# Optimization experiments

Hardware: AMD Instinct MI355X
Metric: run time of the kernel (lower is better)

The kernel has to match this reference:

```python
import jax, jax.numpy as jnp
import numpy as np

M = 16            # num_frequencies
DIM = 512         # dim_input
B = 32768         # flattened batch
H = M + 1         # raw complex table side
N = 2 * M + 1     # autocorrelated table side
NPAR = H * H      # (m+1)^2


def setup_inputs() -> dict:
    key = jax.random.key(0)
    k1, k2, k3 = jax.random.split(key, 3)
    inputs = jax.random.normal(k1, (B, DIM), dtype=jnp.float32)
    targets = jax.random.uniform(k2, (B, 2), dtype=jnp.float32)  # points in [0,1) subset of [-1,1]^2
    # nn.init.normal_(weight, 0.01) => mean=0.01, std=1.0 ; bias zeros
    W = jax.random.normal(k3, (2 * NPAR, DIM), dtype=jnp.float32) + 0.01
    b = jnp.zeros((2 * NPAR,), dtype=jnp.float32)
    return {"inputs": inputs, "targets": targets, "W": W, "b": b}


def reference(inputs, targets, W, b):
    # Linear -> unconstrained complex (m+1)x(m+1) table per sample
    p = inputs @ W.T + b                                   # (B, 2*NPAR)
    real = p[:, :NPAR].reshape(-1, H, H)
    imag = p[:, NPAR:].reshape(-1, H, H)
    seq = jax.lax.complex(real, imag)                      # (B, H, H) complex64

    # 2D linear autocorrelation r[tau] = sum_i seq[i+tau] * conj(seq[i]),
    # tau in [-M, M]^2, via zero-padded FFT (equivalent to the grouped conv2d).
    F = jnp.fft.fft2(seq, s=(N, N))                        # (B, N, N)
    ac = jnp.fft.ifft2(F * jnp.conj(F))                    # circular autocorr
    ac = jnp.roll(ac, (M, M), axis=(-2, -1))               # index a -> lag a-M

    # Normalize so C[0,0] (= centre) equals 1/4 => unit mass on [-1,1]^2
    centre = ac[:, M, M].real                              # sum |seq|^2 > 0
    C = ac / (4.0 * centre)[:, None, None]                 # (B, N, N)

    # Evaluate f(x,y) = sum_{kx,ky} C * exp(i*pi*(kx*x + ky*y))
    k = jnp.arange(-M, M + 1, dtype=jnp.float32)
    kx, ky = jnp.meshgrid(k, k, indexing='xy')             # (N, N)
    tx = targets[:, 0][:, None, None]
    ty = targets[:, 1][:, None, None]
    phase = kx[None] * tx + ky[None] * ty                  # (B, N, N)
    exps = jnp.exp(1j * jnp.pi * phase)
    pdf = jnp.einsum('bij,bij->b', C, exps).real           # (B,)
    return pdf
```

## Files before the change

kernel.cpp:

```cpp
#include <hip/hip_runtime.h>

#define NPARC 289
#define NOUT  578
#define DIMK  512
#define CTILES 40
#define BATCH 32768

typedef __bf16 bf16x8 __attribute__((ext_vector_type(8)));
typedef float floatx4 __attribute__((ext_vector_type(4)));

__device__ __forceinline__ unsigned short f2bf(float f) {
    unsigned u = __float_as_uint(f);
    u = (u + 0x7fffu + ((u >> 16) & 1u)) >> 16;
    return (unsigned short)u;
}

__global__ void prep_w(const float* __restrict__ W, unsigned short* __restrict__ Wp) {
    int wid = threadIdx.x >> 6;
    int lane = threadIdx.x & 63;
    int col = blockIdx.x * 4 + wid;
    int k = lane * 8;
    unsigned short v[8];
    if (col < NOUT) {
        const float* src = W + (size_t)col * DIMK + k;
        #pragma unroll
        for (int j = 0; j < 8; ++j) v[j] = f2bf(src[j]);
    } else {
        #pragma unroll
        for (int j = 0; j < 8; ++j) v[j] = 0;
    }
    int ct = col >> 4;
    int ks = k >> 5;
    int ln = (((k >> 3) & 3) << 4) + (col & 15);
    uint4 o;
    o.x = (unsigned)v[0] | ((unsigned)v[1] << 16);
    o.y = (unsigned)v[2] | ((unsigned)v[3] << 16);
    o.z = (unsigned)v[4] | ((unsigned)v[5] << 16);
    o.w = (unsigned)v[6] | ((unsigned)v[7] << 16);
    *(uint4*)(Wp + (size_t)((ct * 16 + ks) * 64 + ln) * 8) = o;
}

__global__ __launch_bounds__(512, 4) void fused_kernel(
    const float* __restrict__ inputs, const float* __restrict__ targets,
    const float* __restrict__ bias, const unsigned short* __restrict__ Wp,
    float* __restrict__ out)
{
    __shared__ __align__(16) unsigned short Alds[64 * 64 * 8];
    const int tid = threadIdx.x;
    const int base = blockIdx.x * 64;

    const float4* inp4 = (const float4*)(inputs + (size_t)base * DIMK);
    #pragma unroll
    for (int i = 0; i < 16; ++i) {
        int f = i * 512 + tid;
        int s = f >> 7;
        int k = (f & 127) * 4;
        float4 v = inp4[f];
        int t = ((s >> 4) << 4) + (k >> 5);
        int ln = ((((k >> 3) & 3) << 4) + (s & 15)) ^ (t & 7);
        int off = (t * 64 + ln) * 8 + (k & 7);
        union { __bf16 h[4]; uint2 u; } cv;
        cv.h[0] = (__bf16)v.x; cv.h[1] = (__bf16)v.y;
        cv.h[2] = (__bf16)v.z; cv.h[3] = (__bf16)v.w;
        *(uint2*)&Alds[off] = cv.u;
    }
    __syncthreads();

    const int wid  = tid >> 6;
    const int lane = tid & 63;
    const int quad = lane >> 4;
    const int lcol = lane & 15;

    floatx4 acc[5][4];
    #pragma unroll
    for (int t5 = 0; t5 < 5; ++t5)
        #pragma unroll
        for (int st = 0; st < 4; ++st) acc[t5][st] = (floatx4){0.f,0.f,0.f,0.f};

    const bf16x8* Wf = (const bf16x8*)Wp;
    const bf16x8* awp = Wf + ((size_t)(wid * 5 * 16) * 64 + lane);

    #pragma unroll 1
    for (int ks = 0; ks < 16; ++ks) {
        bf16x8 bs[4];
        #pragma unroll
        for (int st = 0; st < 4; ++st) {
            int t = st * 16 + ks;
            bs[st] = *(const bf16x8*)&Alds[(t * 64 + (lane ^ (t & 7))) * 8];
        }
        #pragma unroll
        for (int t5 = 0; t5 < 5; ++t5) {
            bf16x8 aw = awp[(size_t)(t5 * 16 + ks) * 64];
            #pragma unroll
            for (int st = 0; st < 4; ++st)
                acc[t5][st] = __builtin_amdgcn_mfma_f32_16x16x32_bf16(
                    aw, bs[st], acc[t5][st], 0, 0, 0);
        }
    }

    float xs[4], ys[4];
    #pragma unroll
    for (int st = 0; st < 4; ++st) {
        float2 t2 = *(const float2*)(targets + 2 * (base + st * 16 + lcol));
        xs[st] = 0.5f * t2.x;
        ys[st] = 0.5f * t2.y;
    }

    float pd[4]  = {0.f,0.f,0.f,0.f};
    float pr[4]  = {0.f,0.f,0.f,0.f};
    float pim[4] = {0.f,0.f,0.f,0.f};

    #pragma unroll
    for (int t5 = 0; t5 < 5; ++t5)
        #pragma unroll
        for (int reg = 0; reg < 4; ++reg) {
            int colw = (wid * 5 + t5) * 16 + quad * 4 + reg;
            if (colw < NOUT) {
                bool im = (colw >= NPARC);
                int idx = im ? colw - NPARC : colw;
                int r = idx / 17;
                int c = idx - r * 17;
                float cf = (float)c, rf = (float)r;
                float bb = bias[colw];
                #pragma unroll
                for (int st = 0; st < 4; ++st) {
                    float val = acc[t5][st][reg] + bb;
                    float u = fmaf(cf, xs[st], rf * ys[st]);
                    u = __builtin_amdgcn_fractf(u);
                    float sn = __builtin_amdgcn_sinf(u);
                    float cs = __builtin_amdgcn_cosf(u);
                    float a1 = im ? -sn : cs;
                    float a2 = im ?  cs : sn;
                    pd[st]  = fmaf(val, val, pd[st]);
                    pr[st]  = fmaf(val, a1, pr[st]);
                    pim[st] = fmaf(val, a2, pim[st]);
                }
            }
        }

    #pragma unroll
    for (int d = 16; d < 64; d <<= 1)
        #pragma unroll
        for (int st = 0; st < 4; ++st) {
            pd[st]  += __shfl_xor(pd[st], d, 64);
            pr[st]  += __shfl_xor(pr[st], d, 64);
            pim[st] += __shfl_xor(pim[st], d, 64);
        }

    __syncthreads();
    float* R = (float*)Alds;
    if (lane < 16) {
        #pragma unroll
        for (int st = 0; st < 4; ++st) {
            int sl = st * 16 + lane;
            R[(wid * 64 + sl) * 3 + 0] = pd[st];
            R[(wid * 64 + sl) * 3 + 1] = pr[st];
            R[(wid * 64 + sl) * 3 + 2] = pim[st];
        }
    }
    __syncthreads();

    if (tid < 64) {
        float sd = 0.f, sr = 0.f, si = 0.f;
        #pragma unroll
        for (int w = 0; w < 8; ++w) {
            sd += R[(w * 64 + tid) * 3 + 0];
            sr += R[(w * 64 + tid) * 3 + 1];
            si += R[(w * 64 + tid) * 3 + 2];
        }
        out[base + tid] = (sr * sr + si * si) / (4.0f * sd);
    }
}

extern "C" void kernel_launch(void* const* d_in, const int* in_sizes, int n_in,
                              void* d_out, int out_size, void* d_ws, size_t ws_size,
                              hipStream_t stream) {
    const float* inputs  = (const float*)d_in[0];
    const float* targets = (const float*)d_in[1];
    const float* W       = (const float*)d_in[2];
    const float* bias    = (const float*)d_in[3];
    unsigned short* Wp   = (unsigned short*)d_ws;

    prep_w<<<CTILES * 16 / 4, 256, 0, stream>>>(W, Wp);
    fused_kernel<<<BATCH / 64, 512, 0, stream>>>(inputs, targets, bias, Wp, (float*)d_out);
}
```

Baseline: 118.4 us.

## Switch to 32x32 MFMA tiles and feed activations straight from global memory

Replaces the 16x16x32 bf16 MFMA scheme, which staged the 64-sample activation tile through LDS, with 32x32x16 MFMAs. Waves are split into 2 sample halves by 4 column groups. Each lane loads its own sample row from global memory, converts it to bf16 in registers, and prefetches the next k-slice one step ahead. The weight pre-pack is changed to match the 32x32 operand layout. This removes the LDS fill and its barrier, and cuts redundant trig and reduction work per wave. In exchange, each input row is fetched by four waves, each lane does strided uncoalesced row loads, and weight traffic per block doubles.

```diff
diff --git a/kernel.cpp b/kernel.cpp
--- a/kernel.cpp
+++ b/kernel.cpp
@@ -3,11 +3,10 @@
 #define NPARC 289
 #define NOUT  578
 #define DIMK  512
-#define CTILES 40
 #define BATCH 32768
 
 typedef __bf16 bf16x8 __attribute__((ext_vector_type(8)));
-typedef float floatx4 __attribute__((ext_vector_type(4)));
+typedef float floatx16 __attribute__((ext_vector_type(16)));
 
 __device__ __forceinline__ unsigned short f2bf(float f) {
     unsigned u = __float_as_uint(f);
@@ -29,15 +28,16 @@
         #pragma unroll
         for (int j = 0; j < 8; ++j) v[j] = 0;
     }
-    int ct = col >> 4;
-    int ks = k >> 5;
-    int ln = (((k >> 3) & 3) << 4) + (col & 15);
+    int t    = col >> 5;
+    int ks   = lane >> 1;
+    int half = lane & 1;
+    int ln   = half * 32 + (col & 31);
     uint4 o;
     o.x = (unsigned)v[0] | ((unsigned)v[1] << 16);
     o.y = (unsigned)v[2] | ((unsigned)v[3] << 16);
     o.z = (unsigned)v[4] | ((unsigned)v[5] << 16);
     o.w = (unsigned)v[6] | ((unsigned)v[7] << 16);
-    *(uint4*)(Wp + (size_t)((ct * 16 + ks) * 64 + ln) * 8) = o;
+    *(uint4*)(Wp + (size_t)((t * 32 + ks) * 64 + ln) * 8) = o;
 }
 
 __global__ __launch_bounds__(512, 4) void fused_kernel(
@@ -45,128 +45,91 @@
     const float* __restrict__ bias, const unsigned short* __restrict__ Wp,
     float* __restrict__ out)
 {
-    __shared__ __align__(16) unsigned short Alds[64 * 64 * 8];
-    const int tid = threadIdx.x;
-    const int base = blockIdx.x * 64;
-
-    const float4* inp4 = (const float4*)(inputs + (size_t)base * DIMK);
-    #pragma unroll
-    for (int i = 0; i < 16; ++i) {
-        int f = i * 512 + tid;
-        int s = f >> 7;
-        int k = (f & 127) * 4;
-        float4 v = inp4[f];
-        int t = ((s >> 4) << 4) + (k >> 5);
-        int ln = ((((k >> 3) & 3) << 4) + (s & 15)) ^ (t & 7);
-        int off = (t * 64 + ln) * 8 + (k & 7);
-        union { __bf16 h[4]; uint2 u; } cv;
-        cv.h[0] = (__bf16)v.x; cv.h[1] = (__bf16)v.y;
-        cv.h[2] = (__bf16)v.z; cv.h[3] = (__bf16)v.w;
-        *(uint2*)&Alds[off] = cv.u;
-    }
-    __syncthreads();
-
+    __shared__ float R[8][32][3];
+    const int tid  = threadIdx.x;
     const int wid  = tid >> 6;
     const int lane = tid & 63;
-    const int quad = lane >> 4;
-    const int lcol = lane & 15;
+    const int st   = wid & 1;
+    const int g    = wid >> 1;
+    const int base = blockIdx.x * 64;
+    const int sample = base + st * 32 + (lane & 31);
 
-    floatx4 acc[5][4];
+    const float* brow = inputs + (size_t)sample * DIMK + ((lane >> 5) << 3);
+    const bf16x8* awp = (const bf16x8*)Wp + (size_t)(g * 5 * 32) * 64 + lane;
+
+    floatx16 acc[5];
     #pragma unroll
-    for (int t5 = 0; t5 < 5; ++t5)
-        #pragma unroll
-        for (int st = 0; st < 4; ++st) acc[t5][st] = (floatx4){0.f,0.f,0.f,0.f};
+    for (int t5 = 0; t5 < 5; ++t5) acc[t5] = (floatx16)0.f;
 
-    const bf16x8* Wf = (const bf16x8*)Wp;
-    const bf16x8* awp = Wf + ((size_t)(wid * 5 * 16) * 64 + lane);
-
-    #pragma unroll 1
-    for (int ks = 0; ks < 16; ++ks) {
-        bf16x8 bs[4];
-        #pragma unroll
-        for (int st = 0; st < 4; ++st) {
-            int t = st * 16 + ks;
-            bs[st] = *(const bf16x8*)&Alds[(t * 64 + (lane ^ (t & 7))) * 8];
-        }
+    float4 bA = *(const float4*)(brow);
+    float4 bB = *(const float4*)(brow + 4);
+    #pragma unroll 2
+    for (int ks = 0; ks < 32; ++ks) {
+        float4 cA = bA, cB = bB;
+        int nk = (ks + 1) & 31;
+        bA = *(const float4*)(brow + nk * 16);
+        bB = *(const float4*)(brow + nk * 16 + 4);
+        union { __bf16 h[8]; bf16x8 v; } bb;
+        bb.h[0] = (__bf16)cA.x; bb.h[1] = (__bf16)cA.y;
+        bb.h[2] = (__bf16)cA.z; bb.h[3] = (__bf16)cA.w;
+        bb.h[4] = (__bf16)cB.x; bb.h[5] = (__bf16)cB.y;
+        bb.h[6] = (__bf16)cB.z; bb.h[7] = (__bf16)cB.w;
         #pragma unroll
         for (int t5 = 0; t5 < 5; ++t5) {
-            bf16x8 aw = awp[(size_t)(t5 * 16 + ks) * 64];
-            #pragma unroll
-            for (int st = 0; st < 4; ++st)
-                acc[t5][st] = __builtin_amdgcn_mfma_f32_16x16x32_bf16(
-                    aw, bs[st], acc[t5][st], 0, 0, 0);
+            bf16x8 aw = awp[(size_t)(t5 * 32 + ks) * 64];
+            acc[t5] = __builtin_amdgcn_mfma_f32_32x32x16_bf16(aw, bb.v, acc[t5], 0, 0, 0);
         }
     }
 
-    float xs[4], ys[4];
-    #pragma unroll
-    for (int st = 0; st < 4; ++st) {
-        float2 t2 = *(const float2*)(targets + 2 * (base + st * 16 + lcol));
-        xs[st] = 0.5f * t2.x;
-        ys[st] = 0.5f * t2.y;
-    }
+    float2 t2 = *(const float2*)(targets + 2 * sample);
+    float xs = 0.5f * t2.x;
+    float ys = 0.5f * t2.y;
 
-    float pd[4]  = {0.f,0.f,0.f,0.f};
-    float pr[4]  = {0.f,0.f,0.f,0.f};
-    float pim[4] = {0.f,0.f,0.f,0.f};
+    float pd = 0.f, pr = 0.f, pim = 0.f;
 
     #pragma unroll
     for (int t5 = 0; t5 < 5; ++t5)
         #pragma unroll
-        for (int reg = 0; reg < 4; ++reg) {
-            int colw = (wid * 5 + t5) * 16 + quad * 4 + reg;
+        for (int reg = 0; reg < 16; ++reg) {
+            int colw = (g * 5 + t5) * 32 + (reg & 3) + 8 * (reg >> 2) + 4 * (lane >> 5);
             if (colw < NOUT) {
                 bool im = (colw >= NPARC);
                 int idx = im ? colw - NPARC : colw;
                 int r = idx / 17;
                 int c = idx - r * 17;
                 float cf = (float)c, rf = (float)r;
-                float bb = bias[colw];
-                #pragma unroll
-                for (int st = 0; st < 4; ++st) {
-                    float val = acc[t5][st][reg] + bb;
-                    float u = fmaf(cf, xs[st], rf * ys[st]);
-                    u = __builtin_amdgcn_fractf(u);
-                    float sn = __builtin_amdgcn_sinf(u);
-                    float cs = __builtin_amdgcn_cosf(u);
-                    float a1 = im ? -sn : cs;
-                    float a2 = im ?  cs : sn;
-                    pd[st]  = fmaf(val, val, pd[st]);
-                    pr[st]  = fmaf(val, a1, pr[st]);
-                    pim[st] = fmaf(val, a2, pim[st]);
-                }
+                float val = acc[t5][reg] + bias[colw];
+                float u = fmaf(cf, xs, rf * ys);
+                u = __builtin_amdgcn_fractf(u);
+                float sn = __builtin_amdgcn_sinf(u);
+                float cs = __builtin_amdgcn_cosf(u);
+                float a1 = im ? -sn : cs;
+                float a2 = im ?  cs : sn;
+                pd  = fmaf(val, val, pd);
+                pr  = fmaf(val, a1, pr);
+                pim = fmaf(val, a2, pim);
             }
         }
 
-    #pragma unroll
-    for (int d = 16; d < 64; d <<= 1)
-        #pragma unroll
-        for (int st = 0; st < 4; ++st) {
-            pd[st]  += __shfl_xor(pd[st], d, 64);
-            pr[st]  += __shfl_xor(pr[st], d, 64);
-            pim[st] += __shfl_xor(pim[st], d, 64);
-        }
+    pd  += __shfl_xor(pd, 32, 64);
+    pr  += __shfl_xor(pr, 32, 64);
+    pim += __shfl_xor(pim, 32, 64);
 
-    __syncthreads();
-    float* R = (float*)Alds;
-    if (lane < 16) {
-        #pragma unroll
-        for (int st = 0; st < 4; ++st) {
-            int sl = st * 16 + lane;
-            R[(wid * 64 + sl) * 3 + 0] = pd[st];
-            R[(wid * 64 + sl) * 3 + 1] = pr[st];
-            R[(wid * 64 + sl) * 3 + 2] = pim[st];
-        }
+    if (lane < 32) {
+        R[wid][lane][0] = pd;
+        R[wid][lane][1] = pr;
+        R[wid][lane][2] = pim;
     }
     __syncthreads();
 
     if (tid < 64) {
+        int s5 = tid >> 5, j = tid & 31;
         float sd = 0.f, sr = 0.f, si = 0.f;
         #pragma unroll
-        for (int w = 0; w < 8; ++w) {
-            sd += R[(w * 64 + tid) * 3 + 0];
-            sr += R[(w * 64 + tid) * 3 + 1];
-            si += R[(w * 64 + tid) * 3 + 2];
+        for (int gg = 0; gg < 4; ++gg) {
+            sd += R[gg * 2 + s5][j][0];
+            sr += R[gg * 2 + s5][j][1];
+            si += R[gg * 2 + s5][j][2];
         }
         out[base + tid] = (sr * sr + si * si) / (4.0f * sd);
     }
@@ -181,6 +144,6 @@
     const float* bias    = (const float*)d_in[3];
     unsigned short* Wp   = (unsigned short*)d_ws;
 
-    prep_w<<<CTILES * 16 / 4, 256, 0, stream>>>(W, Wp);
+    prep_w<<<160, 256, 0, stream>>>(W, Wp);
     fused_kernel<<<BATCH / 64, 512, 0, stream>>>(inputs, targets, bias, Wp, (float*)d_out);
 }
```

Result: slower. 158.6 us (+33.9%).

## Double-buffer input K-tiles in LDS and interleave real/imag weight columns

Applied to the files above, without the earlier changes.

The kernel now streams the input tile through LDS in four K-chunks with double buffering. Global loads for the next chunk and the next LDS/W fragments are prefetched while MFMAs run on the current ones, which is meant to hide load latency behind compute. prep_w interleaves the real and imag weight rows, so each thread gets matching real/imag pairs and computes sin/cos once per pair, halving transcendental work in the epilogue. Launch bounds drop from 4 to 2 blocks per SM, and the extra register pressure and barriers may reduce occupancy.

```diff
diff --git a/kernel.cpp b/kernel.cpp
--- a/kernel.cpp
+++ b/kernel.cpp
@@ -3,7 +3,6 @@
 #define NPARC 289
 #define NOUT  578
 #define DIMK  512
-#define CTILES 40
 #define BATCH 32768
 
 typedef __bf16 bf16x8 __attribute__((ext_vector_type(8)));
@@ -18,85 +17,84 @@
 __global__ void prep_w(const float* __restrict__ W, unsigned short* __restrict__ Wp) {
     int wid = threadIdx.x >> 6;
     int lane = threadIdx.x & 63;
-    int col = blockIdx.x * 4 + wid;
+    int slot = blockIdx.x * 4 + wid;
     int k = lane * 8;
     unsigned short v[8];
-    if (col < NOUT) {
-        const float* src = W + (size_t)col * DIMK + k;
+    if (slot < NOUT) {
+        int o = (slot & 1) ? NPARC + (slot >> 1) : (slot >> 1);
+        const float* src = W + (size_t)o * DIMK + k;
         #pragma unroll
         for (int j = 0; j < 8; ++j) v[j] = f2bf(src[j]);
     } else {
         #pragma unroll
         for (int j = 0; j < 8; ++j) v[j] = 0;
     }
-    int ct = col >> 4;
+    int ct = slot >> 4;
     int ks = k >> 5;
-    int ln = (((k >> 3) & 3) << 4) + (col & 15);
-    uint4 o;
-    o.x = (unsigned)v[0] | ((unsigned)v[1] << 16);
-    o.y = (unsigned)v[2] | ((unsigned)v[3] << 16);
-    o.z = (unsigned)v[4] | ((unsigned)v[5] << 16);
-    o.w = (unsigned)v[6] | ((unsigned)v[7] << 16);
-    *(uint4*)(Wp + (size_t)((ct * 16 + ks) * 64 + ln) * 8) = o;
-}
-
-__global__ __launch_bounds__(512, 4) void fused_kernel(
+    int ln = (((k >> 3) & 3) << 4) + (slot & 15);
+    uint4 o4;
+    o4.x = (unsigned)v[0] | ((unsigned)v[1] << 16);
+    o4.y = (unsigned)v[2] | ((unsigned)v[3] << 16);
+    o4.z = (unsigned)v[4] | ((unsigned)v[5] << 16);
+    o4.w = (unsigned)v[6] | ((unsigned)v[7] << 16);
+    *(uint4*)(Wp + (size_t)((ct * 16 + ks) * 64 + ln) * 8) = o4;
+}
+
+__global__ __launch_bounds__(512, 2) void fused_kernel(
     const float* __restrict__ inputs, const float* __restrict__ targets,
     const float* __restrict__ bias, const unsigned short* __restrict__ Wp,
     float* __restrict__ out)
 {
-    __shared__ __align__(16) unsigned short Alds[64 * 64 * 8];
-    const int tid = threadIdx.x;
+    __shared__ __align__(16) unsigned short buf[2][64][16][8];
+    __shared__ float R[8][64][3];
+    const int tid  = threadIdx.x;
     const int base = blockIdx.x * 64;
-
-    const float4* inp4 = (const float4*)(inputs + (size_t)base * DIMK);
-    #pragma unroll
-    for (int i = 0; i < 16; ++i) {
-        int f = i * 512 + tid;
-        int s = f >> 7;
-        int k = (f & 127) * 4;
-        float4 v = inp4[f];
-        int t = ((s >> 4) << 4) + (k >> 5);
-        int ln = ((((k >> 3) & 3) << 4) + (s & 15)) ^ (t & 7);
-        int off = (t * 64 + ln) * 8 + (k & 7);
-        union { __bf16 h[4]; uint2 u; } cv;
-        cv.h[0] = (__bf16)v.x; cv.h[1] = (__bf16)v.y;
-        cv.h[2] = (__bf16)v.z; cv.h[3] = (__bf16)v.w;
-        *(uint2*)&Alds[off] = cv.u;
-    }
-    __syncthreads();
-
     const int wid  = tid >> 6;
     const int lane = tid & 63;
     const int quad = lane >> 4;
     const int lcol = lane & 15;
-
-    floatx4 acc[5][4];
-    #pragma unroll
-    for (int t5 = 0; t5 < 5; ++t5)
-        #pragma unroll
-        for (int st = 0; st < 4; ++st) acc[t5][st] = (floatx4){0.f,0.f,0.f,0.f};
-
-    const bf16x8* Wf = (const bf16x8*)Wp;
-    const bf16x8* awp = Wf + ((size_t)(wid * 5 * 16) * 64 + lane);
-
-    #pragma unroll 1
-    for (int ks = 0; ks < 16; ++ks) {
-        bf16x8 bs[4];
-        #pragma unroll
-        for (int st = 0; st < 4; ++st) {
-            int t = st * 16 + ks;
-            bs[st] = *(const bf16x8*)&Alds[(t * 64 + (lane ^ (t & 7))) * 8];
-        }
-        #pragma unroll
-        for (int t5 = 0; t5 < 5; ++t5) {
-            bf16x8 aw = awp[(size_t)(t5 * 16 + ks) * 64];
-            #pragma unroll
-            for (int st = 0; st < 4; ++st)
-                acc[t5][st] = __builtin_amdgcn_mfma_f32_16x16x32_bf16(
-                    aw, bs[st], acc[t5][st], 0, 0, 0);
-        }
-    }
+    const int ct0  = wid * 5;
+
+    const int ss = tid >> 3;
+    const int su = tid & 7;
+    const float4* sp = (const float4*)(inputs + (size_t)(base + ss) * DIMK + su * 16);
+    const int slot0 = (2 * su)     ^ (ss & 7);
+    const int slot1 = (2 * su + 1) ^ (ss & 7);
+
+    float4 g0, g1, g2, g3;
+
+#define WRITE_STAGE(nb) do {                                                  \
+    union { __bf16 h[8]; uint4 u; } c0_, c1_;                                 \
+    c0_.h[0]=(__bf16)g0.x; c0_.h[1]=(__bf16)g0.y;                             \
+    c0_.h[2]=(__bf16)g0.z; c0_.h[3]=(__bf16)g0.w;                             \
+    c0_.h[4]=(__bf16)g1.x; c0_.h[5]=(__bf16)g1.y;                             \
+    c0_.h[6]=(__bf16)g1.z; c0_.h[7]=(__bf16)g1.w;                             \
+    c1_.h[0]=(__bf16)g2.x; c1_.h[1]=(__bf16)g2.y;                             \
+    c1_.h[2]=(__bf16)g2.z; c1_.h[3]=(__bf16)g2.w;                             \
+    c1_.h[4]=(__bf16)g3.x; c1_.h[5]=(__bf16)g3.y;                             \
+    c1_.h[6]=(__bf16)g3.z; c1_.h[7]=(__bf16)g3.w;                             \
+    *(uint4*)&buf[nb][ss][slot0][0] = c0_.u;                                  \
+    *(uint4*)&buf[nb][ss][slot1][0] = c1_.u;                                  \
+} while (0)
+
+#define LDBS(dst, bb, kss)                                                    \
+    { _Pragma("unroll") for (int st_ = 0; st_ < 4; ++st_)                     \
+        dst[st_] = *(const bf16x8*)&buf[bb][st_ * 16 + lcol]                  \
+                       [((kss) * 4 + quad) ^ (lcol & 7)][0]; }
+
+#define LDAW(dst, ksg)                                                        \
+    { _Pragma("unroll") for (int t5_ = 0; t5_ < 5; ++t5_)                     \
+        dst[t5_] = Wf[((size_t)(ct0 + t5_) * 16 + (ksg)) * 64 + lane]; }
+
+#define DOMFMA(aww, bss)                                                      \
+    { _Pragma("unroll") for (int t5_ = 0; t5_ < 5; ++t5_)                     \
+        { _Pragma("unroll") for (int st_ = 0; st_ < 4; ++st_)                 \
+            acc[t5_][st_] = __builtin_amdgcn_mfma_f32_16x16x32_bf16(          \
+                aww[t5_], bss[st_], acc[t5_][st_], 0, 0, 0); } }
+
+    g0 = sp[0]; g1 = sp[1]; g2 = sp[2]; g3 = sp[3];
+    WRITE_STAGE(0);
+    __syncthreads();
 
     float xs[4], ys[4];
     #pragma unroll
@@ -106,34 +104,78 @@
         ys[st] = 0.5f * t2.y;
     }
 
-    float pd[4]  = {0.f,0.f,0.f,0.f};
-    float pr[4]  = {0.f,0.f,0.f,0.f};
-    float pim[4] = {0.f,0.f,0.f,0.f};
-
+    floatx4 acc[5][4];
     #pragma unroll
     for (int t5 = 0; t5 < 5; ++t5)
         #pragma unroll
-        for (int reg = 0; reg < 4; ++reg) {
-            int colw = (wid * 5 + t5) * 16 + quad * 4 + reg;
+        for (int st = 0; st < 4; ++st) acc[t5][st] = (floatx4){0.f, 0.f, 0.f, 0.f};
+
+    const bf16x8* Wf = (const bf16x8*)Wp;
+
+    bf16x8 bsP[4], awP[5], bsQ[4], awQ[5];
+    LDBS(bsP, 0, 0);
+    LDAW(awP, 0);
+
+    #pragma unroll
+    for (int kt = 0; kt < 4; ++kt) {
+        const int cur = kt & 1;
+        if (kt < 3) {
+            g0 = sp[(kt + 1) * 32 + 0];
+            g1 = sp[(kt + 1) * 32 + 1];
+            g2 = sp[(kt + 1) * 32 + 2];
+            g3 = sp[(kt + 1) * 32 + 3];
+        }
+        #pragma unroll
+        for (int ks = 0; ks < 4; ++ks) {
+            const int ksg = kt * 4 + ks;
+            if (ksg & 1) {
+                if (ks < 3)      { LDBS(bsP, cur, ks + 1); LDAW(awP, ksg + 1); }
+                else if (kt < 3) { LDAW(awP, ksg + 1); }
+                DOMFMA(awQ, bsQ);
+            } else {
+                if (ks < 3)      { LDBS(bsQ, cur, ks + 1); LDAW(awQ, ksg + 1); }
+                else if (kt < 3) { LDAW(awQ, ksg + 1); }
+                DOMFMA(awP, bsP);
+            }
+        }
+        __syncthreads();
+        if (kt < 3) {
+            WRITE_STAGE(1 - cur);
+            __syncthreads();
+            LDBS(bsP, 1 - cur, 0);
+        }
+    }
+
+    float pd[4]  = {0.f, 0.f, 0.f, 0.f};
+    float pr[4]  = {0.f, 0.f, 0.f, 0.f};
+    float pim[4] = {0.f, 0.f, 0.f, 0.f};
+
+    #pragma unroll
+    for (int t5 = 0; t5 < 5; ++t5)
+        #pragma unroll
+        for (int p = 0; p < 2; ++p) {
+            int colw = (ct0 + t5) * 16 + quad * 4 + 2 * p;
             if (colw < NOUT) {
-                bool im = (colw >= NPARC);
-                int idx = im ? colw - NPARC : colw;
-                int r = idx / 17;
-                int c = idx - r * 17;
+                int j = colw >> 1;
+                int r = j / 17;
+                int c = j - r * 17;
                 float cf = (float)c, rf = (float)r;
-                float bb = bias[colw];
+                float be = bias[j];
+                float bo = bias[j + NPARC];
                 #pragma unroll
                 for (int st = 0; st < 4; ++st) {
-                    float val = acc[t5][st][reg] + bb;
+                    float ve = acc[t5][st][2 * p]     + be;
+                    float vo = acc[t5][st][2 * p + 1] + bo;
                     float u = fmaf(cf, xs[st], rf * ys[st]);
                     u = __builtin_amdgcn_fractf(u);
                     float sn = __builtin_amdgcn_sinf(u);
                     float cs = __builtin_amdgcn_cosf(u);
-                    float a1 = im ? -sn : cs;
-                    float a2 = im ?  cs : sn;
-                    pd[st]  = fmaf(val, val, pd[st]);
-                    pr[st]  = fmaf(val, a1, pr[st]);
-                    pim[st] = fmaf(val, a2, pim[st]);
+                    pd[st]  = fmaf(ve, ve, pd[st]);
+                    pd[st]  = fmaf(vo, vo, pd[st]);
+                    pr[st]  = fmaf(ve, cs, pr[st]);
+                    pr[st]  = fmaf(-vo, sn, pr[st]);
+                    pim[st] = fmaf(ve, sn, pim[st]);
+                    pim[st] = fmaf(vo, cs, pim[st]);
                 }
             }
         }
@@ -147,15 +189,13 @@
             pim[st] += __shfl_xor(pim[st], d, 64);
         }
 
-    __syncthreads();
-    float* R = (float*)Alds;
     if (lane < 16) {
         #pragma unroll
         for (int st = 0; st < 4; ++st) {
             int sl = st * 16 + lane;
-            R[(wid * 64 + sl) * 3 + 0] = pd[st];
-            R[(wid * 64 + sl) * 3 + 1] = pr[st];
-            R[(wid * 64 + sl) * 3 + 2] = pim[st];
+            R[wid][sl][0] = pd[st];
+            R[wid][sl][1] = pr[st];
+            R[wid][sl][2] = pim[st];
         }
     }
     __syncthreads();
@@ -164,12 +204,16 @@
         float sd = 0.f, sr = 0.f, si = 0.f;
         #pragma unroll
         for (int w = 0; w < 8; ++w) {
-            sd += R[(w * 64 + tid) * 3 + 0];
-            sr += R[(w * 64 + tid) * 3 + 1];
-            si += R[(w * 64 + tid) * 3 + 2];
+            sd += R[w][tid][0];
+            sr += R[w][tid][1];
+            si += R[w][tid][2];
         }
         out[base + tid] = (sr * sr + si * si) / (4.0f * sd);
     }
+#undef WRITE_STAGE
+#undef LDBS
+#undef LDAW
+#undef DOMFMA
 }
 
 extern "C" void kernel_launch(void* const* d_in, const int* in_sizes, int n_in,
@@ -181,6 +225,6 @@
     const float* bias    = (const float*)d_in[3];
     unsigned short* Wp   = (unsigned short*)d_ws;
 
-    prep_w<<<CTILES * 16 / 4, 256, 0, stream>>>(W, Wp);
+    prep_w<<<160, 256, 0, stream>>>(W, Wp);
     fused_kernel<<<BATCH / 64, 512, 0, stream>>>(inputs, targets, bias, Wp, (float*)d_out);
 }
```

Result: slower. 121.2 us (+2.4%).
